# Optimization experiments

Measured on AMD Instinct MI355X. Metric: run time of the kernel, lower is better.

The kernel has to match this reference:

```python
import jax, jax.numpy as jnp
import numpy as np

B, S, D = 1, 2048, 4096
NH, NKV, HD = 32, 8, 128
ROPE_BASE = 500000.0
NEG = -1e30


def apply_rope(x):
    # x: [B, S, H, HD]; interleaved-pair rotary (Llama/torchtune style)
    pos = jnp.arange(x.shape[1], dtype=jnp.float32)
    inv_freq = ROPE_BASE ** (-jnp.arange(0, HD, 2, dtype=jnp.float32) / HD)  # [HD/2]
    ang = pos[:, None] * inv_freq[None, :]            # [S, HD/2]
    cos = jnp.cos(ang)[None, :, None, :]              # [1, S, 1, HD/2]
    sin = jnp.sin(ang)[None, :, None, :]
    xr = x.reshape(x.shape[0], x.shape[1], x.shape[2], HD // 2, 2)
    x0, x1 = xr[..., 0], xr[..., 1]
    out = jnp.stack([x0 * cos - x1 * sin, x0 * sin + x1 * cos], axis=-1)
    return out.reshape(x.shape).astype(x.dtype)


def setup_inputs() -> dict:
    key = jax.random.key(0)
    ks = jax.random.split(key, 5)
    sc = 1.0 / np.sqrt(D).astype(np.float32)
    return {
        "x": jax.random.normal(ks[0], (B, S, D), jnp.float32),
        "Wq": jax.random.normal(ks[1], (D, NH * HD), jnp.float32) * sc,
        "Wk": jax.random.normal(ks[2], (D, NKV * HD), jnp.float32) * sc,
        "Wv": jax.random.normal(ks[3], (D, NKV * HD), jnp.float32) * sc,
        "Wo": jax.random.normal(ks[4], (D, D), jnp.float32) * sc,
    }


def reference(x, Wq, Wk, Wv, Wo):
    # QKV projections (no bias; attention_bias=False)
    q = (x @ Wq).reshape(B, S, NH, HD)      # [B,S,NH,HD]
    k = (x @ Wk).reshape(B, S, NKV, HD)     # [B,S,NKV,HD]
    v = (x @ Wv).reshape(B, S, NKV, HD)
    # RoPE on q and k
    q = apply_rope(q)
    k = apply_rope(k)
    # GQA: group q heads over kv heads instead of materializing expanded k/v
    g = NH // NKV
    qg = q.reshape(B, S, NKV, g, HD)
    scale = 1.0 / np.sqrt(HD).astype(np.float32)
    scores = jnp.einsum('bsngh,btnh->bngst', qg, k) * scale  # [B,NKV,g,S,S]
    causal = jnp.tril(jnp.ones((S, S), dtype=bool))
    scores = jnp.where(causal, scores, NEG)
    p = jax.nn.softmax(scores, axis=-1)
    o = jnp.einsum('bngst,btnh->bsngh', p, v).reshape(B, S, NH * HD)
    return o @ Wo
```

## Files before the change

### kernel.cpp

```cpp
#include <hip/hip_runtime.h>
#include <cstdint>

#define S_LEN 2048
#define D_DIM 4096
#define NHEAD 32
#define NKVH  8
#define HDIM  128
#define NQKV  6144

typedef __bf16 bf16x8 __attribute__((ext_vector_type(8)));
typedef float floatx4 __attribute__((ext_vector_type(4)));
typedef unsigned short u16;
typedef unsigned int u32;

__device__ __forceinline__ u16 f2bf(float f) {
  u32 u = __builtin_bit_cast(u32, f);
  u += 0x7fffu + ((u >> 16) & 1u);
  return (u16)(u >> 16);
}
__device__ __forceinline__ float bf2f(u16 h) {
  u32 u = ((u32)h) << 16;
  return __builtin_bit_cast(float, u);
}

__device__ __forceinline__ void gll16(const void* g, const void* l) {
  __builtin_amdgcn_global_load_lds(
      (const __attribute__((address_space(1))) u32*)(unsigned long long)(uintptr_t)g,
      (__attribute__((address_space(3))) u32*)(u32)(uintptr_t)l, 16, 0, 0);
}


__global__ __launch_bounds__(256) void prep_kernel(const float* __restrict__ x,
                                                   const float* __restrict__ Wq,
                                                   const float* __restrict__ Wk,
                                                   const float* __restrict__ Wv,
                                                   const float* __restrict__ Wo,
                                                   u16* __restrict__ x_bf,
                                                   u16* __restrict__ wqkvT,
                                                   u16* __restrict__ woT) {
  int id = blockIdx.x;
  if (id < 8192) {
    int i = (id * 256 + (int)threadIdx.x) * 4;
    float4 v = *(const float4*)(x + i);
    u32 lo = (u32)f2bf(v.x) | ((u32)f2bf(v.y) << 16);
    u32 hi = (u32)f2bf(v.z) | ((u32)f2bf(v.w) << 16);
    *(uint2*)(x_bf + i) = make_uint2(lo, hi);
    return;
  }
  id -= 8192;
  __shared__ float tile[64][65];
  const float* src;
  u16* dst;
  int N;
  if (id < 4096) {
    src = Wq; dst = wqkvT; N = 4096;
  } else if (id < 5120) {
    src = Wk; dst = wqkvT + (size_t)4096 * 4096; N = 1024; id -= 4096;
  } else if (id < 6144) {
    src = Wv; dst = wqkvT + (size_t)5120 * 4096; N = 1024; id -= 5120;
  } else {
    src = Wo; dst = woT; N = 4096; id -= 6144;
  }
  const int nb = id / 64, kb = id % 64;
  const int k0 = kb * 64, n0 = nb * 64;
  const int t = threadIdx.x;
  const int c4 = (t & 15) * 4, r0 = t >> 4;
#pragma unroll
  for (int p = 0; p < 4; ++p) {
    int r = r0 + p * 16;
    float4 v = *(const float4*)(src + (size_t)(k0 + r) * N + n0 + c4);
    tile[r][c4 + 0] = v.x;
    tile[r][c4 + 1] = v.y;
    tile[r][c4 + 2] = v.z;
    tile[r][c4 + 3] = v.w;
  }
  __syncthreads();
#pragma unroll
  for (int p = 0; p < 4; ++p) {
    int rr = r0 + p * 16;
    u32 a = (u32)f2bf(tile[c4 + 0][rr]) | ((u32)f2bf(tile[c4 + 1][rr]) << 16);
    u32 b = (u32)f2bf(tile[c4 + 2][rr]) | ((u32)f2bf(tile[c4 + 3][rr]) << 16);
    *(uint2*)(dst + (size_t)(n0 + rr) * 4096 + k0 + c4) = make_uint2(a, b);
  }
}

__global__ __launch_bounds__(256) void rope_vt_kernel(u16* __restrict__ qkv,
                                                      u16* __restrict__ vt) {
  int id = blockIdx.x;
  __shared__ u16 tile[64][65];
  if (id < 20480) {
    const int y = id >> 11, s = id & 2047;
    const int sub = threadIdx.x >> 6;
    const int i = threadIdx.x & 63;
    const int hh = y * 4 + sub;
    const int colbase = (hh < NHEAD) ? hh * HDIM : D_DIM + (hh - NHEAD) * HDIM;
    u32* p = (u32*)(qkv + (size_t)s * NQKV + colbase) + i;
    u32 pr = *p;
    float x0 = bf2f((u16)(pr & 0xffffu));
    float x1 = bf2f((u16)(pr >> 16));
    float invf = expf(-(float)(2 * i) * (13.122363377404328f / 128.0f));
    float ang = (float)s * invf;
    float cs = cosf(ang), sn = sinf(ang);
    float o0 = x0 * cs - x1 * sn;
    float o1 = x0 * sn + x1 * cs;
    *p = (u32)f2bf(o0) | ((u32)f2bf(o1) << 16);
    return;
  }
  const int vb = id - 20480;
  const int hk = vb >> 6;
  const int d0 = ((vb >> 5) & 1) * 64;
  const int s0 = (vb & 31) * 64;
  const int t = threadIdx.x, c = t & 63, r0 = t >> 6;
#pragma unroll
  for (int p = 0; p < 16; ++p) {
    int r = r0 + p * 4;
    tile[r][c] = qkv[(size_t)(s0 + r) * NQKV + 5120 + hk * HDIM + d0 + c];
  }
  __syncthreads();
#pragma unroll
  for (int p = 0; p < 16; ++p) {
    int rr = r0 + p * 4;
    vt[((size_t)hk * HDIM + d0 + rr) * S_LEN + s0 + c] = tile[c][rr];
  }
}


template <bool BF16_OUT>
__global__ __launch_bounds__(256) void gemm_bt(const u16* __restrict__ A,
                                               const u16* __restrict__ Bt,
                                               void* __restrict__ Cout,
                                               int M, int N, int K, int lda, int ldb) {
  __shared__ u16 As[2][128 * 32];
  __shared__ u16 Bs[2][128 * 32];
  const int tid = threadIdx.x;
  const int w = tid >> 6, lane = tid & 63;
  const int quad = lane >> 4, l15 = lane & 15;
  const int m0 = blockIdx.y * 128, n0 = blockIdx.x * 128;
  const int wm = (w & 1) * 64, wn = (w >> 1) * 64;
  floatx4 acc[4][4];
#pragma unroll
  for (int mi = 0; mi < 4; ++mi)
#pragma unroll
    for (int ni = 0; ni < 4; ++ni)
#pragma unroll
      for (int j = 0; j < 4; ++j) acc[mi][ni][j] = 0.0f;

  const int srow = w * 32 + (lane >> 2);
  const int kcol = (lane & 3) * 8;
  const u16* pA0 = A + (size_t)(m0 + srow) * lda + kcol;
  const u16* pA1 = pA0 + (size_t)16 * lda;
  const u16* pB0 = Bt + (size_t)(n0 + srow) * ldb + kcol;
  const u16* pB1 = pB0 + (size_t)16 * ldb;

  for (int k0 = 0; k0 < K; k0 += 64) {
#pragma unroll
    for (int c = 0; c < 2; ++c) {
      gll16(pA0 + k0 + c * 32, As[c] + (w * 32) * 32);
      gll16(pA1 + k0 + c * 32, As[c] + (w * 32 + 16) * 32);
      gll16(pB0 + k0 + c * 32, Bs[c] + (w * 32) * 32);
      gll16(pB1 + k0 + c * 32, Bs[c] + (w * 32 + 16) * 32);
    }
    __syncthreads();
#pragma unroll
    for (int c2 = 0; c2 < 2; ++c2) {
      bf16x8 a[4], b[4];
#pragma unroll
      for (int mi = 0; mi < 4; ++mi)
        a[mi] = *(const bf16x8*)(As[c2] + (wm + mi * 16 + l15) * 32 + quad * 8);
#pragma unroll
      for (int ni = 0; ni < 4; ++ni)
        b[ni] = *(const bf16x8*)(Bs[c2] + (wn + ni * 16 + l15) * 32 + quad * 8);
#pragma unroll
      for (int mi = 0; mi < 4; ++mi)
#pragma unroll
        for (int ni = 0; ni < 4; ++ni)
          acc[mi][ni] = __builtin_amdgcn_mfma_f32_16x16x32_bf16(a[mi], b[ni], acc[mi][ni], 0, 0, 0);
    }
    __syncthreads();
  }
#pragma unroll
  for (int mi = 0; mi < 4; ++mi)
#pragma unroll
    for (int ni = 0; ni < 4; ++ni) {
      int row = m0 + wm + mi * 16 + quad * 4;
      int col = n0 + wn + ni * 16 + l15;
#pragma unroll
      for (int j = 0; j < 4; ++j) {
        if (BF16_OUT)
          ((u16*)Cout)[(size_t)(row + j) * N + col] = f2bf(acc[mi][ni][j]);
        else
          ((float*)Cout)[(size_t)(row + j) * N + col] = acc[mi][ni][j];
      }
    }
}


__global__ __launch_bounds__(256) void attn_kernel(const u16* __restrict__ qkv,
                                                   const u16* __restrict__ vt,
                                                   u16* __restrict__ attn_o) {
  __shared__ u16 Ks[4][64 * 32];
  __shared__ u16 Vs[2][128 * 32];
  __shared__ u16 Ps[4][16 * 64];
  const int tid = threadIdx.x, w = tid >> 6, lane = tid & 63;
  const int quad = lane >> 4, l15 = lane & 15;
  const int h = blockIdx.y, hk = h >> 2;
  const int bx = (h & 16) ? blockIdx.x : (gridDim.x - 1 - blockIdx.x);
  const int qb = bx * 128;
  const int mq0 = qb + w * 32;
  const float scale2 = 0.12751744591813488f;
  const int sw = (l15 & 7) * 8;

  bf16x8 qfrag[2][4];
#pragma unroll
  for (int g = 0; g < 2; ++g) {
    const u16* qp = qkv + (size_t)(mq0 + g * 16 + l15) * NQKV + h * HDIM + quad * 8;
#pragma unroll
    for (int c = 0; c < 4; ++c) qfrag[g][c] = *(const bf16x8*)(qp + c * 32);
  }

  floatx4 o[2][8];
#pragma unroll
  for (int g = 0; g < 2; ++g)
#pragma unroll
    for (int nf = 0; nf < 8; ++nf)
#pragma unroll
      for (int j = 0; j < 4; ++j) o[g][nf][j] = 0.0f;
  float m_[2] = {-1e30f, -1e30f}, l_[2] = {0.0f, 0.0f};

  const int nkt = 2 * bx + 2;
  const int srow = lane >> 2;
  const int scol = (lane & 3) * 8;
  const u16* kst = qkv + (size_t)(w * 16 + srow) * NQKV + (D_DIM + hk * HDIM) + scol;
  const u16* vst0 = vt + ((size_t)hk * HDIM + w * 32 + srow) * S_LEN + scol;
  const u16* vst1 = vst0 + (size_t)16 * S_LEN;

  for (int kt = 0; kt < nkt; ++kt) {
    const int kb = kt * 64;
#pragma unroll
    for (int c = 0; c < 4; ++c)
      gll16(kst + (size_t)kb * NQKV + c * 32, &Ks[c][(w * 16) * 32]);
#pragma unroll
    for (int c = 0; c < 2; ++c) {
      gll16(vst0 + kb + c * 32, &Vs[c][(w * 32) * 32]);
      gll16(vst1 + kb + c * 32, &Vs[c][(w * 32 + 16) * 32]);
    }
    __syncthreads();

    if (kb <= mq0) {
      floatx4 sn[2][4];
#pragma unroll
      for (int g = 0; g < 2; ++g)
#pragma unroll
        for (int ki = 0; ki < 4; ++ki)
#pragma unroll
          for (int j = 0; j < 4; ++j) sn[g][ki][j] = 0.0f;
#pragma unroll
      for (int ki = 0; ki < 4; ++ki) {
        if (kb + ki * 16 <= mq0 + 31) {
          const bool g0on = (kb + ki * 16 <= mq0 + 15);
#pragma unroll
          for (int c = 0; c < 4; ++c) {
            bf16x8 kf = *(const bf16x8*)(&Ks[c][(ki * 16 + l15) * 32 + quad * 8]);
            sn[1][ki] = __builtin_amdgcn_mfma_f32_16x16x32_bf16(kf, qfrag[1][c], sn[1][ki], 0, 0, 0);
            if (g0on)
              sn[0][ki] = __builtin_amdgcn_mfma_f32_16x16x32_bf16(kf, qfrag[0][c], sn[0][ki], 0, 0, 0);
          }
        }
      }
      float alw[2];
      bf16x8 pa[2][2];
#pragma unroll
      for (int g = 0; g < 2; ++g) {
        const int qrow = mq0 + g * 16 + l15;
        const int qmax = mq0 + g * 16 + 15;
        float v[16];
        float mv = -1e30f;
#pragma unroll
        for (int ki = 0; ki < 4; ++ki) {
          if (kb + ki * 16 <= qmax) {
#pragma unroll
            for (int dj = 0; dj < 4; ++dj) {
              int key = kb + ki * 16 + quad * 4 + dj;
              float s = sn[g][ki][dj] * scale2;
              float vv = (key > qrow) ? -1e30f : s;
              v[ki * 4 + dj] = vv;
              mv = fmaxf(mv, vv);
            }
          } else {
#pragma unroll
            for (int dj = 0; dj < 4; ++dj) v[ki * 4 + dj] = -1e30f;
          }
        }
        mv = fmaxf(mv, __shfl_xor(mv, 16, 64));
        mv = fmaxf(mv, __shfl_xor(mv, 32, 64));
        float mn = fmaxf(m_[g], mv);
        float a_ = exp2f(m_[g] - mn);
        m_[g] = mn;
        float ps = 0.0f;
#pragma unroll
        for (int ki = 0; ki < 4; ++ki) {
          const int cs = (ki * 16 + quad * 4) ^ sw;
          if (kb + ki * 16 <= qmax) {
            float p0 = exp2f(v[ki * 4 + 0] - mn);
            float p1 = exp2f(v[ki * 4 + 1] - mn);
            float p2 = exp2f(v[ki * 4 + 2] - mn);
            float p3 = exp2f(v[ki * 4 + 3] - mn);
            ps += (p0 + p1) + (p2 + p3);
            u32 pk0 = (u32)f2bf(p0) | ((u32)f2bf(p1) << 16);
            u32 pk1 = (u32)f2bf(p2) | ((u32)f2bf(p3) << 16);
            *(uint2*)(&Ps[w][l15 * 64 + cs]) = make_uint2(pk0, pk1);
          } else {
            *(uint2*)(&Ps[w][l15 * 64 + cs]) = make_uint2(0u, 0u);
          }
        }
        ps += __shfl_xor(ps, 16, 64);
        ps += __shfl_xor(ps, 32, 64);
        l_[g] = l_[g] * a_ + ps;
        alw[g] = a_;
#pragma unroll
        for (int c2 = 0; c2 < 2; ++c2) {
          const int cs = (c2 * 32 + quad * 8) ^ sw;
          pa[g][c2] = *(const bf16x8*)(&Ps[w][l15 * 64 + cs]);
        }
      }
#pragma unroll
      for (int g = 0; g < 2; ++g) {
        float al[4];
#pragma unroll
        for (int dj = 0; dj < 4; ++dj) al[dj] = __shfl(alw[g], quad * 4 + dj, 16);
#pragma unroll
        for (int nf = 0; nf < 8; ++nf)
#pragma unroll
          for (int dj = 0; dj < 4; ++dj) o[g][nf][dj] *= al[dj];
      }
#pragma unroll
      for (int nf = 0; nf < 8; ++nf) {
        bf16x8 vb0 = *(const bf16x8*)(&Vs[0][(nf * 16 + l15) * 32 + quad * 8]);
        bf16x8 vb1 = *(const bf16x8*)(&Vs[1][(nf * 16 + l15) * 32 + quad * 8]);
#pragma unroll
        for (int g = 0; g < 2; ++g) {
          o[g][nf] = __builtin_amdgcn_mfma_f32_16x16x32_bf16(pa[g][0], vb0, o[g][nf], 0, 0, 0);
          o[g][nf] = __builtin_amdgcn_mfma_f32_16x16x32_bf16(pa[g][1], vb1, o[g][nf], 0, 0, 0);
        }
      }
    }
    __syncthreads();
  }

#pragma unroll
  for (int g = 0; g < 2; ++g) {
    float linv = 1.0f / l_[g];
    float rl[4];
#pragma unroll
    for (int dj = 0; dj < 4; ++dj) rl[dj] = __shfl(linv, quad * 4 + dj, 16);
#pragma unroll
    for (int nf = 0; nf < 8; ++nf)
#pragma unroll
      for (int dj = 0; dj < 4; ++dj) {
        int row = mq0 + g * 16 + quad * 4 + dj;
        int col = h * HDIM + nf * 16 + l15;
        attn_o[(size_t)row * D_DIM + col] = f2bf(o[g][nf][dj] * rl[dj]);
      }
  }
}


extern "C" void kernel_launch(void* const* d_in, const int* in_sizes, int n_in,
                              void* d_out, int out_size, void* d_ws, size_t ws_size,
                              hipStream_t stream) {
  const float* x  = (const float*)d_in[0];
  const float* Wq = (const float*)d_in[1];
  const float* Wk = (const float*)d_in[2];
  const float* Wv = (const float*)d_in[3];
  const float* Wo = (const float*)d_in[4];
  float* out = (float*)d_out;
  char* ws = (char*)d_ws;
  const size_t MB = 1024 * 1024;
  u16* x_bf   = (u16*)(ws);
  u16* wqkvT  = (u16*)(ws + 16 * MB);
  u16* woT    = (u16*)(ws + 64 * MB);
  u16* qkv    = (u16*)(ws + 96 * MB);
  u16* vt     = (u16*)(ws + 120 * MB);
  u16* attn_o = (u16*)(ws + 124 * MB);

  prep_kernel<<<8192 + 10240, 256, 0, stream>>>(x, Wq, Wk, Wv, Wo, x_bf, wqkvT, woT);
  gemm_bt<true><<<dim3(48, 16), 256, 0, stream>>>(x_bf, wqkvT, qkv, S_LEN, NQKV, D_DIM, D_DIM, D_DIM);
  rope_vt_kernel<<<20480 + 512, 256, 0, stream>>>(qkv, vt);
  attn_kernel<<<dim3(S_LEN / 128, NHEAD), 256, 0, stream>>>(qkv, vt, attn_o);
  gemm_bt<false><<<dim3(32, 16), 256, 0, stream>>>(attn_o, woT, out, S_LEN, D_DIM, D_DIM, D_DIM, D_DIM);
}
```

Baseline: 556.3 us.

## Restructure attention kernel: 8 waves, double-buffered K/V, lazy softmax rescale

Rewrites the attention kernel to use 512 threads, with each wave owning 16 query rows instead of 32. K/V tiles are double-buffered in swizzled LDS so the next tile's global-to-LDS loads overlap the current compute, and only one barrier is used per iteration. The kernel also skips the online-softmax rescale of the output when the row max grows by less than a threshold, folds the scale into an fma before exp2, uses hardware bf16 packing, and raises wave priority around the MFMA sections. In exchange it uses more LDS per block and doubles the thread count, which may limit occupancy, and the lazy rescale relies on the threshold keeping exp2 values in range.

```diff
diff --git a/kernel.cpp b/kernel.cpp
--- a/kernel.cpp
+++ b/kernel.cpp
@@ -9,6 +9,7 @@
 #define NQKV  6144
 
 typedef __bf16 bf16x8 __attribute__((ext_vector_type(8)));
+typedef __bf16 bf16x2 __attribute__((ext_vector_type(2)));
 typedef float floatx4 __attribute__((ext_vector_type(4)));
 typedef unsigned short u16;
 typedef unsigned int u32;
@@ -21,6 +22,12 @@
 __device__ __forceinline__ float bf2f(u16 h) {
   u32 u = ((u32)h) << 16;
   return __builtin_bit_cast(float, u);
+}
+__device__ __forceinline__ u32 pack2(float a, float b) {
+  bf16x2 t;
+  t[0] = (__bf16)a;
+  t[1] = (__bf16)b;
+  return __builtin_bit_cast(u32, t);
 }
 
 __device__ __forceinline__ void gll16(const void* g, const void* l) {
@@ -83,6 +90,7 @@
     *(uint2*)(dst + (size_t)(n0 + rr) * 4096 + k0 + c4) = make_uint2(a, b);
   }
 }
+
 
 __global__ __launch_bounds__(256) void rope_vt_kernel(u16* __restrict__ qkv,
                                                       u16* __restrict__ vt) {
@@ -195,173 +203,189 @@
 }
 
 
-__global__ __launch_bounds__(256) void attn_kernel(const u16* __restrict__ qkv,
-                                                   const u16* __restrict__ vt,
-                                                   u16* __restrict__ attn_o) {
-  __shared__ u16 Ks[4][64 * 32];
-  __shared__ u16 Vs[2][128 * 32];
-  __shared__ u16 Ps[4][16 * 64];
+__global__ __launch_bounds__(512, 4) void attn_kernel(const u16* __restrict__ qkv,
+                                                      const u16* __restrict__ vt,
+                                                      u16* __restrict__ attn_o) {
+  __shared__ u16 Ks[2][64 * 128];
+  __shared__ u16 Vs[2][128 * 64];
+  __shared__ u16 Ps[8][16 * 64];
   const int tid = threadIdx.x, w = tid >> 6, lane = tid & 63;
   const int quad = lane >> 4, l15 = lane & 15;
   const int h = blockIdx.y, hk = h >> 2;
   const int bx = (h & 16) ? blockIdx.x : (gridDim.x - 1 - blockIdx.x);
   const int qb = bx * 128;
-  const int mq0 = qb + w * 32;
+  const int mq0 = qb + w * 16;
+  const int qrow = mq0 + l15;
   const float scale2 = 0.12751744591813488f;
-  const int sw = (l15 & 7) * 8;
-
-  bf16x8 qfrag[2][4];
-#pragma unroll
-  for (int g = 0; g < 2; ++g) {
-    const u16* qp = qkv + (size_t)(mq0 + g * 16 + l15) * NQKV + h * HDIM + quad * 8;
-#pragma unroll
-    for (int c = 0; c < 4; ++c) qfrag[g][c] = *(const bf16x8*)(qp + c * 32);
-  }
-
-  floatx4 o[2][8];
-#pragma unroll
-  for (int g = 0; g < 2; ++g)
-#pragma unroll
-    for (int nf = 0; nf < 8; ++nf)
-#pragma unroll
-      for (int j = 0; j < 4; ++j) o[g][nf][j] = 0.0f;
-  float m_[2] = {-1e30f, -1e30f}, l_[2] = {0.0f, 0.0f};
+  const int xsw = (l15 & 7) * 8;
+
+  bf16x8 qfrag[4];
+  {
+    const u16* qp = qkv + (size_t)qrow * NQKV + h * HDIM + quad * 8;
+#pragma unroll
+    for (int c = 0; c < 4; ++c) qfrag[c] = *(const bf16x8*)(qp + c * 32);
+  }
+
+  floatx4 o[8];
+#pragma unroll
+  for (int nf = 0; nf < 8; ++nf)
+#pragma unroll
+    for (int j = 0; j < 4; ++j) o[nf][j] = 0.0f;
+  float m_ = -1e30f, l_ = 0.0f;
+
+  const int krow0 = w * 8 + (lane >> 4);
+  const int krow1 = krow0 + 4;
+  const int kcol0 = ((lane & 15) * 8) ^ ((krow0 & 7) * 8);
+  const int kcol1 = ((lane & 15) * 8) ^ ((krow1 & 7) * 8);
+  const u16* kg0 = qkv + (size_t)krow0 * NQKV + (D_DIM + hk * HDIM) + kcol0;
+  const u16* kg1 = qkv + (size_t)krow1 * NQKV + (D_DIM + hk * HDIM) + kcol1;
+  const int vd0 = w * 16 + (lane >> 3);
+  const int vd1 = vd0 + 8;
+  const int vcol = ((lane & 7) * 8) ^ (((lane >> 3) & 7) * 8);
+  const u16* vg0 = vt + ((size_t)hk * HDIM + vd0) * S_LEN + vcol;
+  const u16* vg1 = vt + ((size_t)hk * HDIM + vd1) * S_LEN + vcol;
+  const int sofs0 = w * 1024 + lane * 8;
+  const int sofs1 = sofs0 + 512;
 
   const int nkt = 2 * bx + 2;
-  const int srow = lane >> 2;
-  const int scol = (lane & 3) * 8;
-  const u16* kst = qkv + (size_t)(w * 16 + srow) * NQKV + (D_DIM + hk * HDIM) + scol;
-  const u16* vst0 = vt + ((size_t)hk * HDIM + w * 32 + srow) * S_LEN + scol;
-  const u16* vst1 = vst0 + (size_t)16 * S_LEN;
+
+#define STAGE(b, kb2)                                    \
+  do {                                                   \
+    gll16(kg0 + (size_t)(kb2)*NQKV, &Ks[b][sofs0]);      \
+    gll16(kg1 + (size_t)(kb2)*NQKV, &Ks[b][sofs1]);      \
+    gll16(vg0 + (kb2), &Vs[b][sofs0]);                   \
+    gll16(vg1 + (kb2), &Vs[b][sofs1]);                   \
+  } while (0)
+
+  STAGE(0, 0);
+  __syncthreads();
 
   for (int kt = 0; kt < nkt; ++kt) {
     const int kb = kt * 64;
-#pragma unroll
-    for (int c = 0; c < 4; ++c)
-      gll16(kst + (size_t)kb * NQKV + c * 32, &Ks[c][(w * 16) * 32]);
-#pragma unroll
-    for (int c = 0; c < 2; ++c) {
-      gll16(vst0 + kb + c * 32, &Vs[c][(w * 32) * 32]);
-      gll16(vst1 + kb + c * 32, &Vs[c][(w * 32 + 16) * 32]);
+    const int cur = kt & 1;
+    if (kt + 1 < nkt) STAGE(cur ^ 1, kb + 64);
+
+    if (kb <= mq0 + 15) {
+      const u16* ksb = Ks[cur];
+      const u16* vsb = Vs[cur];
+      floatx4 sn[4];
+#pragma unroll
+      for (int ki = 0; ki < 4; ++ki)
+#pragma unroll
+        for (int j = 0; j < 4; ++j) sn[ki][j] = 0.0f;
+
+      __builtin_amdgcn_s_setprio(1);
+#pragma unroll
+      for (int ki = 0; ki < 4; ++ki) {
+        if (kb + ki * 16 <= mq0 + 15) {
+#pragma unroll
+          for (int c = 0; c < 4; ++c) {
+            bf16x8 kf = *(const bf16x8*)(ksb + (ki * 16 + l15) * 128 + ((c * 32 + quad * 8) ^ xsw));
+            sn[ki] = __builtin_amdgcn_mfma_f32_16x16x32_bf16(kf, qfrag[c], sn[ki], 0, 0, 0);
+          }
+        }
+      }
+      __builtin_amdgcn_s_setprio(0);
+
+      float mv = -1e30f;
+      if (kb + 63 <= mq0) {
+#pragma unroll
+        for (int ki = 0; ki < 4; ++ki)
+#pragma unroll
+          for (int j = 0; j < 4; ++j) mv = fmaxf(mv, sn[ki][j]);
+      } else {
+#pragma unroll
+        for (int ki = 0; ki < 4; ++ki) {
+          if (kb + ki * 16 <= mq0 + 15) {
+#pragma unroll
+            for (int j = 0; j < 4; ++j) {
+              int key = kb + ki * 16 + quad * 4 + j;
+              float s = (key <= qrow) ? sn[ki][j] : -1e30f;
+              sn[ki][j] = s;
+              mv = fmaxf(mv, s);
+            }
+          }
+        }
+      }
+      mv = fmaxf(mv, __shfl_xor(mv, 16, 64));
+      mv = fmaxf(mv, __shfl_xor(mv, 32, 64));
+
+      const float THRR = 62.73636f;
+      const bool skip = __all(mv <= m_ + THRR);
+      float a_ = 1.0f, mb;
+      if (skip) {
+        mb = -m_ * scale2;
+      } else {
+        float mn = fmaxf(m_, mv);
+        a_ = exp2f((m_ - mn) * scale2);
+        m_ = mn;
+        mb = -mn * scale2;
+      }
+
+      float ps = 0.0f;
+      u16* psrow = &Ps[w][l15 * 64];
+#pragma unroll
+      for (int ki = 0; ki < 4; ++ki) {
+        uint2 pk;
+        if (kb + ki * 16 <= mq0 + 15) {
+          float p0 = exp2f(fmaf(sn[ki][0], scale2, mb));
+          float p1 = exp2f(fmaf(sn[ki][1], scale2, mb));
+          float p2 = exp2f(fmaf(sn[ki][2], scale2, mb));
+          float p3 = exp2f(fmaf(sn[ki][3], scale2, mb));
+          ps += (p0 + p1) + (p2 + p3);
+          pk.x = pack2(p0, p1);
+          pk.y = pack2(p2, p3);
+        } else {
+          pk = make_uint2(0u, 0u);
+        }
+        *(uint2*)(psrow + ((ki * 16 + quad * 4) ^ xsw)) = pk;
+      }
+      ps += __shfl_xor(ps, 16, 64);
+      ps += __shfl_xor(ps, 32, 64);
+
+      if (skip) {
+        l_ += ps;
+      } else {
+        l_ = l_ * a_ + ps;
+        float al[4];
+#pragma unroll
+        for (int j = 0; j < 4; ++j) al[j] = __shfl(a_, quad * 4 + j, 16);
+#pragma unroll
+        for (int nf = 0; nf < 8; ++nf)
+#pragma unroll
+          for (int j = 0; j < 4; ++j) o[nf][j] *= al[j];
+      }
+
+      bf16x8 pa0 = *(const bf16x8*)(psrow + ((quad * 8) ^ xsw));
+      bf16x8 pa1 = *(const bf16x8*)(psrow + ((32 + quad * 8) ^ xsw));
+
+      __builtin_amdgcn_s_setprio(1);
+#pragma unroll
+      for (int nf = 0; nf < 8; ++nf) {
+        const u16* vrow = vsb + (nf * 16 + l15) * 64;
+        bf16x8 vb0 = *(const bf16x8*)(vrow + ((quad * 8) ^ xsw));
+        bf16x8 vb1 = *(const bf16x8*)(vrow + ((32 + quad * 8) ^ xsw));
+        o[nf] = __builtin_amdgcn_mfma_f32_16x16x32_bf16(pa0, vb0, o[nf], 0, 0, 0);
+        o[nf] = __builtin_amdgcn_mfma_f32_16x16x32_bf16(pa1, vb1, o[nf], 0, 0, 0);
+      }
+      __builtin_amdgcn_s_setprio(0);
     }
     __syncthreads();
-
-    if (kb <= mq0) {
-      floatx4 sn[2][4];
-#pragma unroll
-      for (int g = 0; g < 2; ++g)
-#pragma unroll
-        for (int ki = 0; ki < 4; ++ki)
-#pragma unroll
-          for (int j = 0; j < 4; ++j) sn[g][ki][j] = 0.0f;
-#pragma unroll
-      for (int ki = 0; ki < 4; ++ki) {
-        if (kb + ki * 16 <= mq0 + 31) {
-          const bool g0on = (kb + ki * 16 <= mq0 + 15);
-#pragma unroll
-          for (int c = 0; c < 4; ++c) {
-            bf16x8 kf = *(const bf16x8*)(&Ks[c][(ki * 16 + l15) * 32 + quad * 8]);
-            sn[1][ki] = __builtin_amdgcn_mfma_f32_16x16x32_bf16(kf, qfrag[1][c], sn[1][ki], 0, 0, 0);
-            if (g0on)
-              sn[0][ki] = __builtin_amdgcn_mfma_f32_16x16x32_bf16(kf, qfrag[0][c], sn[0][ki], 0, 0, 0);
-          }
-        }
-      }
-      float alw[2];
-      bf16x8 pa[2][2];
-#pragma unroll
-      for (int g = 0; g < 2; ++g) {
-        const int qrow = mq0 + g * 16 + l15;
-        const int qmax = mq0 + g * 16 + 15;
-        float v[16];
-        float mv = -1e30f;
-#pragma unroll
-        for (int ki = 0; ki < 4; ++ki) {
-          if (kb + ki * 16 <= qmax) {
-#pragma unroll
-            for (int dj = 0; dj < 4; ++dj) {
-              int key = kb + ki * 16 + quad * 4 + dj;
-              float s = sn[g][ki][dj] * scale2;
-              float vv = (key > qrow) ? -1e30f : s;
-              v[ki * 4 + dj] = vv;
-              mv = fmaxf(mv, vv);
-            }
-          } else {
-#pragma unroll
-            for (int dj = 0; dj < 4; ++dj) v[ki * 4 + dj] = -1e30f;
-          }
-        }
-        mv = fmaxf(mv, __shfl_xor(mv, 16, 64));
-        mv = fmaxf(mv, __shfl_xor(mv, 32, 64));
-        float mn = fmaxf(m_[g], mv);
-        float a_ = exp2f(m_[g] - mn);
-        m_[g] = mn;
-        float ps = 0.0f;
-#pragma unroll
-        for (int ki = 0; ki < 4; ++ki) {
-          const int cs = (ki * 16 + quad * 4) ^ sw;
-          if (kb + ki * 16 <= qmax) {
-            float p0 = exp2f(v[ki * 4 + 0] - mn);
-            float p1 = exp2f(v[ki * 4 + 1] - mn);
-            float p2 = exp2f(v[ki * 4 + 2] - mn);
-            float p3 = exp2f(v[ki * 4 + 3] - mn);
-            ps += (p0 + p1) + (p2 + p3);
-            u32 pk0 = (u32)f2bf(p0) | ((u32)f2bf(p1) << 16);
-            u32 pk1 = (u32)f2bf(p2) | ((u32)f2bf(p3) << 16);
-            *(uint2*)(&Ps[w][l15 * 64 + cs]) = make_uint2(pk0, pk1);
-          } else {
-            *(uint2*)(&Ps[w][l15 * 64 + cs]) = make_uint2(0u, 0u);
-          }
-        }
-        ps += __shfl_xor(ps, 16, 64);
-        ps += __shfl_xor(ps, 32, 64);
-        l_[g] = l_[g] * a_ + ps;
-        alw[g] = a_;
-#pragma unroll
-        for (int c2 = 0; c2 < 2; ++c2) {
-          const int cs = (c2 * 32 + quad * 8) ^ sw;
-          pa[g][c2] = *(const bf16x8*)(&Ps[w][l15 * 64 + cs]);
-        }
-      }
-#pragma unroll
-      for (int g = 0; g < 2; ++g) {
-        float al[4];
-#pragma unroll
-        for (int dj = 0; dj < 4; ++dj) al[dj] = __shfl(alw[g], quad * 4 + dj, 16);
-#pragma unroll
-        for (int nf = 0; nf < 8; ++nf)
-#pragma unroll
-          for (int dj = 0; dj < 4; ++dj) o[g][nf][dj] *= al[dj];
-      }
-#pragma unroll
-      for (int nf = 0; nf < 8; ++nf) {
-        bf16x8 vb0 = *(const bf16x8*)(&Vs[0][(nf * 16 + l15) * 32 + quad * 8]);
-        bf16x8 vb1 = *(const bf16x8*)(&Vs[1][(nf * 16 + l15) * 32 + quad * 8]);
-#pragma unroll
-        for (int g = 0; g < 2; ++g) {
-          o[g][nf] = __builtin_amdgcn_mfma_f32_16x16x32_bf16(pa[g][0], vb0, o[g][nf], 0, 0, 0);
-          o[g][nf] = __builtin_amdgcn_mfma_f32_16x16x32_bf16(pa[g][1], vb1, o[g][nf], 0, 0, 0);
-        }
-      }
+  }
+#undef STAGE
+
+  float linv = 1.0f / l_;
+  float rl[4];
+#pragma unroll
+  for (int j = 0; j < 4; ++j) rl[j] = __shfl(linv, quad * 4 + j, 16);
+#pragma unroll
+  for (int nf = 0; nf < 8; ++nf)
+#pragma unroll
+    for (int j = 0; j < 4; ++j) {
+      int row = mq0 + quad * 4 + j;
+      int col = h * HDIM + nf * 16 + l15;
+      attn_o[(size_t)row * D_DIM + col] = f2bf(o[nf][j] * rl[j]);
     }
-    __syncthreads();
-  }
-
-#pragma unroll
-  for (int g = 0; g < 2; ++g) {
-    float linv = 1.0f / l_[g];
-    float rl[4];
-#pragma unroll
-    for (int dj = 0; dj < 4; ++dj) rl[dj] = __shfl(linv, quad * 4 + dj, 16);
-#pragma unroll
-    for (int nf = 0; nf < 8; ++nf)
-#pragma unroll
-      for (int dj = 0; dj < 4; ++dj) {
-        int row = mq0 + g * 16 + quad * 4 + dj;
-        int col = h * HDIM + nf * 16 + l15;
-        attn_o[(size_t)row * D_DIM + col] = f2bf(o[g][nf][dj] * rl[dj]);
-      }
-  }
 }
 
 
@@ -386,6 +410,6 @@
   prep_kernel<<<8192 + 10240, 256, 0, stream>>>(x, Wq, Wk, Wv, Wo, x_bf, wqkvT, woT);
   gemm_bt<true><<<dim3(48, 16), 256, 0, stream>>>(x_bf, wqkvT, qkv, S_LEN, NQKV, D_DIM, D_DIM, D_DIM);
   rope_vt_kernel<<<20480 + 512, 256, 0, stream>>>(qkv, vt);
-  attn_kernel<<<dim3(S_LEN / 128, NHEAD), 256, 0, stream>>>(qkv, vt, attn_o);
+  attn_kernel<<<dim3(S_LEN / 128, NHEAD), 512, 0, stream>>>(qkv, vt, attn_o);
   gemm_bt<false><<<dim3(32, 16), 256, 0, stream>>>(attn_o, woT, out, S_LEN, D_DIM, D_DIM, D_DIM, D_DIM);
 }
```

Result: faster. 496.3 us (-10.8%).
